# Optimization experiments

Measured on AMD Instinct MI355X. Metric: run time of the kernel, lower is better.

The kernel has to match this reference:

```python
import jax, jax.numpy as jnp
import numpy as np

N = 100_000      # nodes
E = 1_600_000    # edges (avg degree 16)
EMB = 32         # embedding_n
VOCAB = 100_000  # nodes_feats_size


def setup_inputs() -> dict:
    key = jax.random.key(0)
    ks = jax.random.split(key, 12)
    s = 1.0 / np.sqrt(EMB)
    return dict(
        features=jax.random.randint(ks[0], (N,), 0, VOCAB),
        cars=jax.random.uniform(ks[1], (N, 1), dtype=jnp.float32),
        entered=jax.random.uniform(ks[2], (N, 1), dtype=jnp.float32),
        free=jax.random.randint(ks[3], (N, 1), 0, 2).astype(jnp.float32),
        src=jax.random.randint(ks[4], (E,), 0, N),
        dst=jax.random.randint(ks[5], (E,), 0, N),
        embed_table=jax.random.normal(ks[6], (VOCAB, EMB), jnp.float32),
        W2n=jax.random.normal(ks[7], (EMB + 1, 1), jnp.float32) * s,
        b2n=jnp.zeros((1,), jnp.float32),
        W2e=jax.random.normal(ks[8], (2 * EMB, EMB), jnp.float32) * s,
        b2e=jnp.zeros((EMB,), jnp.float32),
        W3=jax.random.normal(ks[9], (EMB + 3, 8), jnp.float32) * s,
        b3=jnp.zeros((8,), jnp.float32),
        W4=jax.random.normal(ks[10], (8, 1), jnp.float32) * s,
        b4=jnp.zeros((1,), jnp.float32),
    )


def reference(features, cars, entered, free, src, dst,
              embed_table, W2n, b2n, W2e, b2e, W3, b3, W4, b4):
    relu = jax.nn.relu
    # --- apply_nodes: PredictParkingModule ---
    emb = embed_table[features]                                   # [N, EMB]
    parked = jnp.concatenate([emb, cars], axis=1) @ W2n + b2n     # [N, 1]
    cars1 = relu(relu(parked) + cars)                             # updated 'cars'
    # --- apply_edges: PredictEdgeProbModule ---
    he = jnp.concatenate([emb[src], emb[dst]], axis=1) @ W2e + b2e          # [E, EMB]
    h = relu(jnp.concatenate([he, cars1[src], cars1[dst], entered[src]], axis=1) @ W3 + b3)
    h = h @ W4 + b4                                                          # [E, 1]
    selfloop = (features[src] == features[dst]).astype(jnp.float32)[:, None]  # [E, 1]
    enabled = (selfloop != free[src]).astype(jnp.float32)                     # [E, 1]
    logit = relu(h) * enabled                                                 # [E, 1]
    # --- group_apply_edges(group_by='src'): per-source softmax over edges ---
    l = logit[:, 0]
    m = jax.lax.stop_gradient(jax.ops.segment_max(l, src, num_segments=N))
    ex = jnp.exp(l - m[src])
    ssum = jax.ops.segment_sum(ex, src, num_segments=N)
    prob = (ex / ssum[src])[:, None]                              # [E, 1]
    # --- pull: flow_message_func + flow_reduce_func (sum over dst) ---
    c = cars1[src] * prob                                         # all moving
    o = c * (1.0 - selfloop)                                      # outer
    cars_out = jax.ops.segment_sum(c, dst, num_segments=N)        # [N, 1]
    entered_out = jax.ops.segment_sum(o, dst, num_segments=N)     # [N, 1]
    return cars_out, emb, entered_out
```

## Files before the change

kernel.cpp:

```cpp
#include <hip/hip_runtime.h>
#include <stdint.h>

typedef _Float16 f16x8 __attribute__((ext_vector_type(8)));

#define RBITS 9
#define RSZ   512
#define G     512
#define MAXB  256
#define CHMAX 3200
#define RMAX  7

template<int NT>
__device__ __forceinline__ uint32_t scanExcl(uint32_t v, uint32_t* wtot, int t)
{
    uint32_t x = v;
    #pragma unroll
    for (int d = 1; d < 64; d <<= 1) {
        uint32_t y = __shfl_up(x, d, 64);
        if ((t & 63) >= d) x += y;
    }
    int w = t >> 6;
    if ((t & 63) == 63) wtot[w] = x;
    __syncthreads();
    uint32_t pre = 0;
    #pragma unroll
    for (int k = 0; k < NT / 64; ++k) pre += (k < w) ? wtot[k] : 0;
    return pre + x - v;
}

__global__ __launch_bounds__(512) void nodecount_kernel(
    const int*   __restrict__ features,
    const float* __restrict__ cars,
    const float* __restrict__ entered,
    const float* __restrict__ free_,
    const float* __restrict__ embed_table,
    const float* __restrict__ W2n,
    const float* __restrict__ b2n,
    const float* __restrict__ W2e,
    const float* __restrict__ W3,
    const int* __restrict__ src, const int* __restrict__ dst,
    float* __restrict__ emb_out,
    float* __restrict__ cars1,
    f16x8* __restrict__ Ah,
    f16x8* __restrict__ Bh,
    float* __restrict__ sfree,
    uint16_t* __restrict__ cntS, uint16_t* __restrict__ cntD,
    int N, int E, int B)
{
    __shared__ uint32_t cS[MAXB], cD[MAXB];
    int t = threadIdx.x, g = blockIdx.x;
    for (int i = t; i < MAXB; i += 512) { cS[i] = 0; cD[i] = 0; }
    __syncthreads();
    int per = (E + G - 1) / G;
    int lo = g * per, hi = min(E, lo + per);
    for (int i = lo + t; i < hi; i += 512) {
        atomicAdd(&cS[src[i] >> RBITS], 1u);
        atomicAdd(&cD[dst[i] >> RBITS], 1u);
    }
    __syncthreads();
    for (int i = t; i < B; i += 512) {
        cntS[(size_t)i * G + g] = (uint16_t)cS[i];
        cntD[(size_t)i * G + g] = (uint16_t)cD[i];
    }

    if (g * 512 >= N) return;
    __shared__ float Wa[256], Wb[256];
    if (t < 256) {
        int k = t >> 3, j = t & 7;
        float a = 0.f, b = 0.f;
        #pragma unroll
        for (int m = 0; m < 32; ++m) {
            float w3 = W3[m * 8 + j];
            a += W2e[k * 32 + m]        * w3;
            b += W2e[(32 + k) * 32 + m] * w3;
        }
        Wa[t] = a;
        Wb[t] = b;
    }
    __syncthreads();

    int i = g * 512 + t;
    if (i >= N) return;
    int f = features[i];
    const float4* erow = (const float4*)(embed_table + (size_t)f * 32);
    float4* orow = (float4*)(emb_out + (size_t)i * 32);
    float e[32];
    #pragma unroll
    for (int q = 0; q < 8; ++q) {
        float4 v = erow[q];
        orow[q] = v;
        e[4*q+0] = v.x; e[4*q+1] = v.y; e[4*q+2] = v.z; e[4*q+3] = v.w;
    }
    float parked = b2n[0];
    #pragma unroll
    for (int k = 0; k < 32; ++k) parked += e[k] * W2n[k];
    float c = cars[i];
    parked += c * W2n[32];
    float c1 = fmaxf(fmaxf(parked, 0.f) + c, 0.f);
    cars1[i] = c1;
    float fm = (float)f + 1.f;
    sfree[i] = (free_[i] > 0.5f) ? -fm : fm;

    float ent = entered[i];
    float a8[8], b8[8];
    #pragma unroll
    for (int j = 0; j < 8; ++j) {
        a8[j] = c1 * W3[32*8 + j] + ent * W3[34*8 + j];
        b8[j] = c1 * W3[33*8 + j];
    }
    #pragma unroll
    for (int k = 0; k < 32; ++k) {
        float x = e[k];
        #pragma unroll
        for (int j = 0; j < 8; ++j) {
            a8[j] += x * Wa[k*8 + j];
            b8[j] += x * Wb[k*8 + j];
        }
    }
    f16x8 av, bv;
    #pragma unroll
    for (int j = 0; j < 8; ++j) { av[j] = (_Float16)a8[j]; bv[j] = (_Float16)b8[j]; }
    Ah[i] = av;
    Bh[i] = bv;
}

__global__ __launch_bounds__(512) void scanA_kernel(
    uint16_t* __restrict__ cntS, uint16_t* __restrict__ cntD,
    uint32_t* __restrict__ totS, uint32_t* __restrict__ totD, int B)
{
    __shared__ uint32_t wtot[8];
    int arr = (int)(blockIdx.x >= (unsigned)B);
    int b = blockIdx.x - (arr ? B : 0);
    uint16_t* a   = arr ? cntD : cntS;
    uint32_t* tot = arr ? totD : totS;
    int t = threadIdx.x;
    uint32_t v = a[(size_t)b * G + t];
    uint32_t e = scanExcl<512>(v, wtot, t);
    a[(size_t)b * G + t] = (uint16_t)e;
    if (t == G - 1) tot[b] = e + v;
}

__global__ __launch_bounds__(512) void scatter_kernel(
    const int* __restrict__ src, const int* __restrict__ dst,
    const float* __restrict__ sfree,
    const f16x8* __restrict__ Ah, const f16x8* __restrict__ Bh,
    const float* __restrict__ b2e, const float* __restrict__ W3,
    const float* __restrict__ b3,  const float* __restrict__ W4,
    const float* __restrict__ b4,
    const uint16_t* __restrict__ cntS, const uint16_t* __restrict__ cntD,
    const uint32_t* __restrict__ totS, const uint32_t* __restrict__ totD,
    uint32_t* __restrict__ payloadS,
    uint64_t* __restrict__ metaEx,
    int E, int B)
{
    __shared__ float b3p[8];
    __shared__ uint32_t curS[MAXB], curD[MAXB];
    __shared__ uint32_t tblS[MAXB], tblD[MAXB];
    __shared__ uint32_t wtot[8];
    __shared__ union { uint32_t b32[CHMAX]; uint64_t b64[CHMAX]; } stg;
    __shared__ uint16_t bid[CHMAX];

    int t = threadIdx.x, g = blockIdx.x;
    uint32_t vS = (t < B) ? totS[t] : 0;
    uint32_t eS = scanExcl<512>(vS, wtot, t);
    __syncthreads();
    uint32_t vD = (t < B) ? totD[t] : 0;
    uint32_t eD = scanExcl<512>(vD, wtot, t);
    if (t < B) {
        curS[t] = eS + cntS[(size_t)t * G + g];
        curD[t] = eD + cntD[(size_t)t * G + g];
    }
    if (t < MAXB) { tblS[t] = 0; tblD[t] = 0; }
    if (t < 8) {
        float s = b3[t];
        #pragma unroll
        for (int m = 0; m < 32; ++m) s += b2e[m] * W3[m * 8 + t];
        b3p[t] = s;
    }
    __syncthreads();
    float w4[8]; float bias4 = b4[0];
    #pragma unroll
    for (int j = 0; j < 8; ++j) w4[j] = W4[j];

    int per = (E + G - 1) / G;
    int lo = g * per, hi = min(E, lo + per), n = hi - lo;

    int   sA[RMAX], dA[RMAX];
    #pragma unroll
    for (int r = 0; r < RMAX; ++r) {
        int idx = min(r * 512 + t, n - 1);
        int i = lo + idx;
        sA[r] = src[i];
        dA[r] = dst[i];
    }
    f16x8 avA[RMAX], bvA[RMAX];
    float fsvA[RMAX], fdvA[RMAX];
    #pragma unroll
    for (int r = 0; r < RMAX; ++r) {
        avA[r]  = Ah[sA[r]];
        bvA[r]  = Bh[dA[r]];
        fsvA[r] = sfree[sA[r]];
        fdvA[r] = sfree[dA[r]];
    }

    uint32_t regA[RMAX], regB[RMAX], regC[RMAX];
    #pragma unroll
    for (int r = 0; r < RMAX; ++r) {
        int idx = r * 512 + t;
        int s = sA[r], d = dA[r];
        float out = bias4;
        #pragma unroll
        for (int j = 0; j < 8; ++j)
            out += fmaxf((float)avA[r][j] + (float)bvA[r][j] + b3p[j], 0.f) * w4[j];
        bool self  = (fabsf(fsvA[r]) == fabsf(fdvA[r]));
        bool freeS = (fsvA[r] < 0.f);
        float l = (self != freeS) ? fmaxf(out, 0.f) : 0.f;
        float ex = __expf(l);
        uint32_t exb = (uint32_t)__builtin_bit_cast(unsigned short, (_Float16)ex);
        if (idx < n) {
            uint32_t keyS = (uint32_t)s >> RBITS;
            uint32_t keyD = (uint32_t)d >> RBITS;
            uint32_t rankS = atomicAdd(&tblS[keyS], 1u);
            uint32_t rankD = atomicAdd(&tblD[keyD], 1u);
            regA[r] = keyS | (rankS << 8) | (self ? 0x80000000u : 0u);
            regB[r] = keyD | (rankD << 8) | ((uint32_t)(d & (RSZ - 1)) << 21);
            regC[r] = (uint32_t)(s & (RSZ - 1)) | (exb << 16);
        }
    }
    __syncthreads();
    uint32_t hS = (t < MAXB) ? tblS[t] : 0;
    uint32_t hD = (t < MAXB) ? tblD[t] : 0;
    __syncthreads();
    uint32_t bS = scanExcl<512>(hS, wtot, t);
    __syncthreads();
    uint32_t bD = scanExcl<512>(hD, wtot, t);
    if (t < MAXB) {
        tblS[t] = bS;
        tblD[t] = bD;
    }
    __syncthreads();

    #pragma unroll
    for (int r = 0; r < RMAX; ++r) {
        int idx = r * 512 + t;
        if (idx < n) {
            uint32_t key = regA[r] & 255u;
            uint32_t slot = tblS[key] + ((regA[r] >> 8) & 0xFFFu);
            stg.b32[slot] = regC[r];
            bid[slot] = (uint16_t)key;
        }
    }
    __syncthreads();
    for (int j = t; j < n; j += 512) {
        uint32_t b = bid[j];
        payloadS[curS[b] + (j - tblS[b])] = stg.b32[j];
    }
    __syncthreads();

    #pragma unroll
    for (int r = 0; r < RMAX; ++r) {
        int idx = r * 512 + t;
        if (idx < n) {
            uint32_t key = regB[r] & 255u;
            uint32_t slot = tblD[key] + ((regB[r] >> 8) & 0xFFFu);
            uint32_t s = ((regA[r] & 255u) << RBITS) | (regC[r] & (RSZ - 1));
            uint32_t mlo = s | (((regB[r] >> 21) & 0x1FFu) << 17)
                         | (regA[r] & 0x80000000u);
            stg.b64[slot] = (uint64_t)mlo | ((uint64_t)(regC[r] >> 16) << 32);
            bid[slot] = (uint16_t)key;
        }
    }
    __syncthreads();
    for (int j = t; j < n; j += 512) {
        uint32_t b = bid[j];
        metaEx[curD[b] + (j - tblD[b])] = stg.b64[j];
    }
}

__global__ __launch_bounds__(1024) void bucketS_kernel(
    const uint32_t* __restrict__ totS, const uint32_t* __restrict__ payloadS,
    const float* __restrict__ cars1, float* __restrict__ ratio,
    int N, int B)
{
    __shared__ float acc[RSZ];
    __shared__ uint32_t wtot[16];
    __shared__ uint32_t be[2];
    int b = blockIdx.x, t = threadIdx.x;
    uint32_t v = (t < B) ? totS[t] : 0;
    uint32_t e = scanExcl<1024>(v, wtot, t);
    if (t == b) { be[0] = e; be[1] = e + v; }
    for (int i = t; i < RSZ; i += 1024) acc[i] = 0.f;
    __syncthreads();
    uint32_t beg = be[0], end = be[1];
    for (uint32_t i = beg + t; i < end; i += 1024) {
        uint32_t p = payloadS[i];
        float val = (float)__builtin_bit_cast(_Float16, (unsigned short)(p >> 16));
        atomicAdd(&acc[p & (RSZ - 1)], val);
    }
    __syncthreads();
    int nb = b << RBITS;
    for (int i = t; i < RSZ; i += 1024) {
        int node = nb + i;
        if (node < N) {
            float s = acc[i];
            ratio[node] = cars1[node] / (s > 0.f ? s : 1.f);
        }
    }
}

__global__ __launch_bounds__(1024) void bucketD_kernel(
    const uint32_t* __restrict__ totD,
    const uint64_t* __restrict__ metaEx,
    const float* __restrict__ ratio,
    float* __restrict__ cars_out, float* __restrict__ entered_out,
    int N, int B)
{
    __shared__ float accC[RSZ], accX[RSZ];
    __shared__ uint32_t wtot[16];
    __shared__ uint32_t be[2];
    int b = blockIdx.x, t = threadIdx.x;
    uint32_t v = (t < B) ? totD[t] : 0;
    uint32_t e = scanExcl<1024>(v, wtot, t);
    if (t == b) { be[0] = e; be[1] = e + v; }
    for (int i = t; i < RSZ; i += 1024) { accC[i] = 0.f; accX[i] = 0.f; }
    __syncthreads();
    uint32_t beg = be[0], end = be[1];
    for (uint32_t i = beg + t; i < end; i += 1024) {
        uint64_t me = metaEx[i];
        uint32_t m = (uint32_t)me;
        float ex = (float)__builtin_bit_cast(_Float16, (unsigned short)(me >> 32));
        int s  = m & 0x1FFFF;
        int ld = (m >> 17) & (RSZ - 1);
        float c = ratio[s] * ex;
        atomicAdd(&accC[ld], c);
        if (m & 0x80000000u) atomicAdd(&accX[ld], c);
    }
    __syncthreads();
    int nb = b << RBITS;
    for (int i = t; i < RSZ; i += 1024) {
        int node = nb + i;
        if (node < N) {
            float cs = accC[i];
            cars_out[node]    = cs;
            entered_out[node] = cs - accX[i];
        }
    }
}

extern "C" void kernel_launch(void* const* d_in, const int* in_sizes, int n_in,
                              void* d_out, int out_size, void* d_ws, size_t ws_size,
                              hipStream_t stream)
{
    const int N = in_sizes[0];
    const int E = in_sizes[4];
    const int B = (N + RSZ - 1) / RSZ;
    const int L = B * G;

    const int*   features    = (const int*)  d_in[0];
    const float* cars        = (const float*)d_in[1];
    const float* entered     = (const float*)d_in[2];
    const float* free_       = (const float*)d_in[3];
    const int*   src         = (const int*)  d_in[4];
    const int*   dst         = (const int*)  d_in[5];
    const float* embed_table = (const float*)d_in[6];
    const float* W2n         = (const float*)d_in[7];
    const float* b2n         = (const float*)d_in[8];
    const float* W2e         = (const float*)d_in[9];
    const float* b2e         = (const float*)d_in[10];
    const float* W3          = (const float*)d_in[11];
    const float* b3          = (const float*)d_in[12];
    const float* W4          = (const float*)d_in[13];
    const float* b4          = (const float*)d_in[14];

    float* out         = (float*)d_out;
    float* cars_out    = out;
    float* emb_out     = out + N;
    float* entered_out = out + (size_t)N * 33;

    float*    ws       = (float*)d_ws;
    float*    cars1    = ws;
    float*    ratio    = ws + N;
    float*    sfree    = ws + (size_t)2 * N;
    f16x8*    Ah       = (f16x8*)(ws + (size_t)4 * N);
    f16x8*    Bh       = (f16x8*)(ws + (size_t)8 * N);
    uint32_t* totS     = (uint32_t*)(ws + (size_t)12 * N);
    uint32_t* totD     = totS + MAXB;
    uint64_t* metaEx   = (uint64_t*)(totD + MAXB);
    uint32_t* payloadS = (uint32_t*)(metaEx + E);
    uint16_t* cntS     = (uint16_t*)(payloadS + E);
    uint16_t* cntD     = cntS + L;

    nodecount_kernel<<<G, 512, 0, stream>>>(
        features, cars, entered, free_, embed_table, W2n, b2n, W2e, W3,
        src, dst, emb_out, cars1, Ah, Bh, sfree, cntS, cntD, N, E, B);
    scanA_kernel<<<2 * B, 512, 0, stream>>>(cntS, cntD, totS, totD, B);
    scatter_kernel<<<G, 512, 0, stream>>>(
        src, dst, sfree, Ah, Bh, b2e, W3, b3, W4, b4,
        cntS, cntD, totS, totD, payloadS, metaEx, E, B);
    bucketS_kernel<<<B, 1024, 0, stream>>>(totS, payloadS, cars1, ratio, N, B);
    bucketD_kernel<<<B, 1024, 0, stream>>>(
        totD, metaEx, ratio, cars_out, entered_out, N, B);
}
```

Before: 89.52 us.

## Split edge MLP out of scatter into a separate grid-stride kernel

```diff
diff --git a/kernel.cpp b/kernel.cpp
--- a/kernel.cpp
+++ b/kernel.cpp
@@ -124,6 +124,46 @@
     Bh[i] = bv;
 }
 
+__global__ __launch_bounds__(256) void edgemlp_kernel(
+    const int* __restrict__ src, const int* __restrict__ dst,
+    const float* __restrict__ sfree,
+    const f16x8* __restrict__ Ah, const f16x8* __restrict__ Bh,
+    const float* __restrict__ b2e, const float* __restrict__ W3,
+    const float* __restrict__ b3,  const float* __restrict__ W4,
+    const float* __restrict__ b4,
+    uint16_t* __restrict__ exh, int E)
+{
+    __shared__ float b3p[8];
+    if (threadIdx.x < 8) {
+        float s = b3[threadIdx.x];
+        #pragma unroll
+        for (int m = 0; m < 32; ++m) s += b2e[m] * W3[m * 8 + threadIdx.x];
+        b3p[threadIdx.x] = s;
+    }
+    __syncthreads();
+    float w4[8]; float bias4 = b4[0];
+    #pragma unroll
+    for (int j = 0; j < 8; ++j) w4[j] = W4[j];
+
+    int stride = gridDim.x * blockDim.x;
+    for (int e = blockIdx.x * blockDim.x + threadIdx.x; e < E; e += stride) {
+        int s = src[e], d = dst[e];
+        f16x8 av = Ah[s], bv = Bh[d];
+        float fsv = sfree[s];
+        float fdv = sfree[d];
+        float out = bias4;
+        #pragma unroll
+        for (int j = 0; j < 8; ++j)
+            out += fmaxf((float)av[j] + (float)bv[j] + b3p[j], 0.f) * w4[j];
+        bool self  = (fabsf(fsv) == fabsf(fdv));
+        bool freeS = (fsv < 0.f);
+        float l = (self != freeS) ? fmaxf(out, 0.f) : 0.f;
+        float ex = __expf(l);
+        uint16_t exb = __builtin_bit_cast(unsigned short, (_Float16)ex);
+        exh[e] = (uint16_t)(exb | (self ? 0x8000u : 0u));
+    }
+}
+
 __global__ __launch_bounds__(512) void scanA_kernel(
     uint16_t* __restrict__ cntS, uint16_t* __restrict__ cntD,
     uint32_t* __restrict__ totS, uint32_t* __restrict__ totD, int B)
@@ -140,20 +180,15 @@
     if (t == G - 1) tot[b] = e + v;
 }
 
-__global__ __launch_bounds__(512) void scatter_kernel(
+__global__ __launch_bounds__(512) void bin_kernel(
     const int* __restrict__ src, const int* __restrict__ dst,
-    const float* __restrict__ sfree,
-    const f16x8* __restrict__ Ah, const f16x8* __restrict__ Bh,
-    const float* __restrict__ b2e, const float* __restrict__ W3,
-    const float* __restrict__ b3,  const float* __restrict__ W4,
-    const float* __restrict__ b4,
+    const uint16_t* __restrict__ exh,
     const uint16_t* __restrict__ cntS, const uint16_t* __restrict__ cntD,
     const uint32_t* __restrict__ totS, const uint32_t* __restrict__ totD,
     uint32_t* __restrict__ payloadS,
     uint64_t* __restrict__ metaEx,
     int E, int B)
 {
-    __shared__ float b3p[8];
     __shared__ uint32_t curS[MAXB], curD[MAXB];
     __shared__ uint32_t tblS[MAXB], tblD[MAXB];
     __shared__ uint32_t wtot[8];
@@ -171,58 +206,26 @@
         curD[t] = eD + cntD[(size_t)t * G + g];
     }
     if (t < MAXB) { tblS[t] = 0; tblD[t] = 0; }
-    if (t < 8) {
-        float s = b3[t];
-        #pragma unroll
-        for (int m = 0; m < 32; ++m) s += b2e[m] * W3[m * 8 + t];
-        b3p[t] = s;
-    }
-    __syncthreads();
-    float w4[8]; float bias4 = b4[0];
-    #pragma unroll
-    for (int j = 0; j < 8; ++j) w4[j] = W4[j];
+    __syncthreads();
 
     int per = (E + G - 1) / G;
     int lo = g * per, hi = min(E, lo + per), n = hi - lo;
 
-    int   sA[RMAX], dA[RMAX];
-    #pragma unroll
-    for (int r = 0; r < RMAX; ++r) {
-        int idx = min(r * 512 + t, n - 1);
-        int i = lo + idx;
-        sA[r] = src[i];
-        dA[r] = dst[i];
-    }
-    f16x8 avA[RMAX], bvA[RMAX];
-    float fsvA[RMAX], fdvA[RMAX];
-    #pragma unroll
-    for (int r = 0; r < RMAX; ++r) {
-        avA[r]  = Ah[sA[r]];
-        bvA[r]  = Bh[dA[r]];
-        fsvA[r] = sfree[sA[r]];
-        fdvA[r] = sfree[dA[r]];
-    }
-
     uint32_t regA[RMAX], regB[RMAX], regC[RMAX];
     #pragma unroll
     for (int r = 0; r < RMAX; ++r) {
         int idx = r * 512 + t;
-        int s = sA[r], d = dA[r];
-        float out = bias4;
-        #pragma unroll
-        for (int j = 0; j < 8; ++j)
-            out += fmaxf((float)avA[r][j] + (float)bvA[r][j] + b3p[j], 0.f) * w4[j];
-        bool self  = (fabsf(fsvA[r]) == fabsf(fdvA[r]));
-        bool freeS = (fsvA[r] < 0.f);
-        float l = (self != freeS) ? fmaxf(out, 0.f) : 0.f;
-        float ex = __expf(l);
-        uint32_t exb = (uint32_t)__builtin_bit_cast(unsigned short, (_Float16)ex);
         if (idx < n) {
+            int i = lo + idx;
+            int s = src[i], d = dst[i];
+            uint32_t eb = exh[i];
+            uint32_t self = eb >> 15;
+            uint32_t exb  = eb & 0x7FFFu;
             uint32_t keyS = (uint32_t)s >> RBITS;
             uint32_t keyD = (uint32_t)d >> RBITS;
             uint32_t rankS = atomicAdd(&tblS[keyS], 1u);
             uint32_t rankD = atomicAdd(&tblD[keyD], 1u);
-            regA[r] = keyS | (rankS << 8) | (self ? 0x80000000u : 0u);
+            regA[r] = keyS | (rankS << 8) | (self << 31);
             regB[r] = keyD | (rankD << 8) | ((uint32_t)(d & (RSZ - 1)) << 21);
             regC[r] = (uint32_t)(s & (RSZ - 1)) | (exb << 16);
         }
@@ -387,16 +390,18 @@
     uint32_t* totD     = totS + MAXB;
     uint64_t* metaEx   = (uint64_t*)(totD + MAXB);
     uint32_t* payloadS = (uint32_t*)(metaEx + E);
-    uint16_t* cntS     = (uint16_t*)(payloadS + E);
+    uint16_t* exh      = (uint16_t*)(payloadS + E);
+    uint16_t* cntS     = exh + E;
     uint16_t* cntD     = cntS + L;
 
     nodecount_kernel<<<G, 512, 0, stream>>>(
         features, cars, entered, free_, embed_table, W2n, b2n, W2e, W3,
         src, dst, emb_out, cars1, Ah, Bh, sfree, cntS, cntD, N, E, B);
+    edgemlp_kernel<<<2048, 256, 0, stream>>>(
+        src, dst, sfree, Ah, Bh, b2e, W3, b3, W4, b4, exh, E);
     scanA_kernel<<<2 * B, 512, 0, stream>>>(cntS, cntD, totS, totD, B);
-    scatter_kernel<<<G, 512, 0, stream>>>(
-        src, dst, sfree, Ah, Bh, b2e, W3, b3, W4, b4,
-        cntS, cntD, totS, totD, payloadS, metaEx, E, B);
+    bin_kernel<<<G, 512, 0, stream>>>(
+        src, dst, exh, cntS, cntD, totS, totD, payloadS, metaEx, E, B);
     bucketS_kernel<<<B, 1024, 0, stream>>>(totS, payloadS, cars1, ratio, N, B);
     bucketD_kernel<<<B, 1024, 0, stream>>>(
         totD, metaEx, ratio, cars_out, entered_out, N, B);
```

Result: slower. 94.44 us (+5.5%).
